# Kernel optimization log

Measured on AMD Instinct MI355X. Metric: run time of the kernel, lower is better.

## Reference

```python
import jax, jax.numpy as jnp
import numpy as np

B, T, U = 64, 512, 1024
TIME_STEP = 0.008

# Rieke cone phototransduction parameters (scaleFac = 1, values are final)
PR = dict(sigma=22.0, phi=22.0, eta=2000.0, beta=9.0, cgmp2cur=0.01,
          cgmphill=3.0, cdark=1.0, betaSlow=0.4, hillcoef=4.0,
          hillaffinity=0.5, gamma=10.0, gdark=20.0)


def setup_inputs() -> dict:
    key = jax.random.key(0)
    X = jax.random.uniform(key, (B, T, U), dtype=jnp.float32)  # light intensity >= 0
    inp = {"X_fun": X}
    for name, v in PR.items():
        inp[name] = jnp.full((1, U), v, dtype=jnp.float32)  # flax param shape (1, units)
    return inp


def reference(X_fun, sigma, phi, eta, beta, cgmp2cur, cgmphill, cdark,
              betaSlow, hillcoef, hillaffinity, gamma, gdark):
    # Derived constants (as in runRiekeModel preamble)
    darkCurrent = gdark ** cgmphill * cgmp2cur / 2
    gdark_e = (2 * darkCurrent / cgmp2cur) ** (1 / cgmphill)
    cur2ca = beta * cdark / darkCurrent
    smax = eta / phi * gdark_e * (1 + (cdark / hillaffinity) ** hillcoef)

    Bd, Td, Ud = X_fun.shape
    ones = jnp.ones((Bd, Ud), X_fun.dtype)
    g0 = gdark_e * ones
    s0 = gdark_e * eta / phi * ones
    c0 = cdark * ones
    cslow0 = cdark * ones
    r0 = X_fun[:, 0, :] * gamma / sigma
    p0 = (eta + r0) / phi

    def step(carry, x_prev):
        g, s, c, cslow, p, r = carry
        r_n = r + TIME_STEP * (-sigma * r) + gamma * x_prev
        p_n = p + TIME_STEP * (r + eta - phi * p)
        c_n = c + TIME_STEP * (cur2ca * cgmp2cur * g ** cgmphill
                               / (1 + cslow / cdark) - beta * c)
        cslow_n = cslow - TIME_STEP * (betaSlow * (cslow - c))
        s_n = smax / (1 + (c_n / hillaffinity) ** hillcoef)
        g_n = g + TIME_STEP * (s - p * g)
        return (g_n, s_n, c_n, cslow_n, p_n, r_n), g_n

    xs = jnp.moveaxis(X_fun[:, :-1, :], 1, 0)  # [T-1, B, U], step pnt uses X[:, pnt-1, :]
    _, g_seq = jax.lax.scan(step, (g0, s0, c0, cslow0, p0, r0), xs)
    # g[:, 0, :] stays zero in the original (loop starts at pnt=1)
    g = jnp.concatenate([jnp.zeros((Bd, 1, Ud), X_fun.dtype),
                         jnp.moveaxis(g_seq, 0, 1)], axis=1)
    return -(cgmp2cur * g ** cgmphill) / 2
```

## Files before the change

kernel.cpp:

```cpp
#include <hip/hip_runtime.h>
#include <math.h>


#define TT 512
#define UU 1024
#define UN 16
#define DTSTEP 0.008f

__device__ __forceinline__ void gload_lds(const float* g, float* l) {
    __builtin_amdgcn_global_load_lds(
        (__attribute__((address_space(1))) void*)(uintptr_t)g,
        (__attribute__((address_space(3))) void*)l, 4, 0, 0);
}

template <bool FAST>
__device__ __forceinline__ void run_chain(
    const float* __restrict__ xrow, float* __restrict__ orow,
    float* __restrict__ swave,
    int lane,
    float sigma, float phi, float eta, float beta, float cgmp2cur,
    float cgmphill, float cdark, float betaSlow, float hillcoef,
    float hillaff, float gam, float gdark)
{
    const float darkCurrent = powf(gdark, cgmphill) * cgmp2cur * 0.5f;
    const float gdark_e = powf(2.0f * darkCurrent / cgmp2cur, 1.0f / cgmphill);
    const float cur2ca = beta * cdark / darkCurrent;
    const float smax = eta / phi * gdark_e *
                       (1.0f + powf(cdark / hillaff, hillcoef));

    const float Ar   = 1.0f - DTSTEP * sigma;
    const float icd  = 1.0f / cdark;
    const float kc   = cur2ca * cgmp2cur;
    const float iha  = 1.0f / hillaff;
    const float outk = -0.5f * cgmp2cur;
    const float dtbs = DTSTEP * betaSlow;

    float g  = gdark_e;
    float s  = gdark_e * eta / phi;
    float c  = cdark;
    float cs = cdark;
    float r, p;
    {
        float x0 = xrow[0];
        r = x0 * gam / sigma;
        p = (eta + r) / phi;
    }
    float gp = FAST ? g * g * g : __powf(g, cgmphill);

    orow[0] = 0.0f;

    auto step = [&](float x, float& outv) {
        float rn  = fmaf(Ar, r, gam * x);
        float pn  = fmaf(DTSTEP, (r + eta) - phi * p, p);
        float den = fmaf(cs, icd, 1.0f);
        float cn  = fmaf(DTSTEP,
                         fmaf(-beta, c, kc * gp * __builtin_amdgcn_rcpf(den)),
                         c);
        float csn = fmaf(-dtbs, cs - c, cs);
        float sn;
        if (FAST) {
            float t2 = cn * iha;
            t2 *= t2;
            sn = smax * __builtin_amdgcn_rcpf(fmaf(t2, t2, 1.0f));
        } else {
            sn = smax / (1.0f + __powf(cn * iha, hillcoef));
        }
        float gn  = fmaf(DTSTEP, fmaf(-p, g, s), g);
        float gpn = FAST ? gn * gn * gn : __powf(gn, cgmphill);
        outv = outk * gpn;
        g = gn; s = sn; c = cn; cs = csn; p = pn; r = rn; gp = gpn;
    };

#pragma unroll
    for (int k = 0; k < UN; ++k)
        gload_lds(xrow + k * UU, swave + k * 64);

    const float* xst = xrow + UN * UU;
    float* op = orow + UU;

    for (int n = 0; n < TT / UN - 1; ++n) {
        if (n == 0) {
            asm volatile("s_waitcnt vmcnt(0)" ::: "memory");
        } else {
            asm volatile("s_waitcnt vmcnt(16)" ::: "memory");
        }
        __builtin_amdgcn_sched_barrier(0);
        const int p2 = (n & 1) * (UN * 64);
        float xa[UN];
#pragma unroll
        for (int k = 0; k < UN; ++k) xa[k] = swave[p2 + k * 64 + lane];
        __builtin_amdgcn_sched_barrier(0);
        const int q2 = ((n & 1) ^ 1) * (UN * 64);
#pragma unroll
        for (int k = 0; k < UN; ++k)
            gload_lds(xst + k * UU, swave + q2 + k * 64);
        __builtin_amdgcn_sched_barrier(0);
#pragma unroll
        for (int k = 0; k < UN; ++k) {
            float o;
            step(xa[k], o);
            op[k * UU] = o;
        }
        xst += UN * UU;
        op += UN * UU;
    }

    asm volatile("s_waitcnt vmcnt(16)" ::: "memory");
    __builtin_amdgcn_sched_barrier(0);
    {
        const int p2 = (31 & 1) * (UN * 64);
        float xa[UN];
#pragma unroll
        for (int k = 0; k < UN; ++k) xa[k] = swave[p2 + k * 64 + lane];
#pragma unroll
        for (int k = 0; k < UN - 1; ++k) {
            float o;
            step(xa[k], o);
            op[k * UU] = o;
        }
    }
}

__global__ __launch_bounds__(256, 1) void prfr_kernel(
    const float* __restrict__ X,
    const float* __restrict__ sigma_p, const float* __restrict__ phi_p,
    const float* __restrict__ eta_p,   const float* __restrict__ beta_p,
    const float* __restrict__ cgmp2cur_p, const float* __restrict__ cgmphill_p,
    const float* __restrict__ cdark_p, const float* __restrict__ betaSlow_p,
    const float* __restrict__ hillcoef_p, const float* __restrict__ hillaff_p,
    const float* __restrict__ gamma_p, const float* __restrict__ gdark_p,
    float* __restrict__ out, int total)
{
    __shared__ float smem[4][2][UN][64];

    const int idx = blockIdx.x * blockDim.x + threadIdx.x;
    if (idx >= total) return;
    const int u = idx & (UU - 1);
    const int b = idx >> 10;
    const int w = __builtin_amdgcn_readfirstlane(threadIdx.x >> 6);
    const int lane = threadIdx.x & 63;

    const float* xrow = X + (long)b * (TT * UU) + u;
    float* orow = out + (long)b * (TT * UU) + u;

    const float sigma = sigma_p[u], phi = phi_p[u], eta = eta_p[u];
    const float beta = beta_p[u], cgmp2cur = cgmp2cur_p[u];
    const float cgmphill = cgmphill_p[u], cdark = cdark_p[u];
    const float betaSlow = betaSlow_p[u], hillcoef = hillcoef_p[u];
    const float hillaff = hillaff_p[u], gam = gamma_p[u], gdark = gdark_p[u];

    float* swave = &smem[w][0][0][0];

    if (cgmphill == 3.0f && hillcoef == 4.0f) {
        run_chain<true>(xrow, orow, swave, lane, sigma, phi, eta, beta,
                        cgmp2cur, cgmphill, cdark, betaSlow, hillcoef,
                        hillaff, gam, gdark);
    } else {
        run_chain<false>(xrow, orow, swave, lane, sigma, phi, eta, beta,
                         cgmp2cur, cgmphill, cdark, betaSlow, hillcoef,
                         hillaff, gam, gdark);
    }
}

extern "C" void kernel_launch(void* const* d_in, const int* in_sizes, int n_in,
                              void* d_out, int out_size, void* d_ws, size_t ws_size,
                              hipStream_t stream)
{
    const float* X = (const float*)d_in[0];
    const int B = in_sizes[0] / (TT * UU);
    const int total = B * UU;
    const int block = 256;
    const int grid = (total + block - 1) / block;
    prfr_kernel<<<grid, block, 0, stream>>>(
        X,
        (const float*)d_in[1],  (const float*)d_in[2],  (const float*)d_in[3],
        (const float*)d_in[4],  (const float*)d_in[5],  (const float*)d_in[6],
        (const float*)d_in[7],  (const float*)d_in[8],  (const float*)d_in[9],
        (const float*)d_in[10], (const float*)d_in[11], (const float*)d_in[12],
        (float*)d_out, total);
}
```

Measured before the change: 257.3 us.

## Stage inputs with 16-byte LDS loads and fold step constants

The fast path now stages X into LDS with 16-byte global_load_lds transfers instead of 4-byte ones, remapping lanes so each wave fetches four timesteps per instruction. This cuts staging instructions per 16-step chunk from 16 to 4. The step's constants are pre-folded (P1, Ke, KC, C1), which shortens the serial dependency chain slightly. Output addressing uses a 32-bit unsigned offset, and the phase loop is unrolled by two. The generic path becomes a plain loop, and waitcnt counts still assume in-order completion alongside the stores.

```diff
diff --git a/kernel.cpp b/kernel.cpp
--- a/kernel.cpp
+++ b/kernel.cpp
@@ -4,20 +4,118 @@
 
 #define TT 512
 #define UU 1024
-#define UN 16
 #define DTSTEP 0.008f
 
-__device__ __forceinline__ void gload_lds(const float* g, float* l) {
+__device__ __forceinline__ void gload16(const float* g, float* l) {
     __builtin_amdgcn_global_load_lds(
         (__attribute__((address_space(1))) void*)(uintptr_t)g,
-        (__attribute__((address_space(3))) void*)l, 4, 0, 0);
-}
-
-template <bool FAST>
-__device__ __forceinline__ void run_chain(
-    const float* __restrict__ xrow, float* __restrict__ orow,
-    float* __restrict__ swave,
-    int lane,
+        (__attribute__((address_space(3))) void*)l, 16, 0, 0);
+}
+
+__device__ __forceinline__ void run_fast(
+    const float* __restrict__ xrow, float* __restrict__ out, unsigned ob,
+    const float* gstage, float* __restrict__ wlds, int lane,
+    float sigma, float phi, float eta, float beta, float cgmp2cur,
+    float cdark, float betaSlow, float hillaff, float gam, float gdark)
+{
+    const float darkCurrent = gdark * gdark * gdark * cgmp2cur * 0.5f;
+    const float gdark_e = gdark;
+    const float cur2ca = beta * cdark / darkCurrent;
+    const float ha2 = (cdark / hillaff) * (cdark / hillaff);
+    const float smax = eta / phi * gdark_e * (1.0f + ha2 * ha2);
+
+    const float Ar   = 1.0f - DTSTEP * sigma;
+    const float P1   = 1.0f - DTSTEP * phi;
+    const float Ke   = DTSTEP * eta;
+    const float icd  = 1.0f / cdark;
+    const float KC   = DTSTEP * cur2ca * cgmp2cur;
+    const float C1   = 1.0f - DTSTEP * beta;
+    const float dtbs = DTSTEP * betaSlow;
+    const float iha  = 1.0f / hillaff;
+    const float outk = -0.5f * cgmp2cur;
+
+    float g  = gdark_e;
+    float s  = gdark_e * eta / phi;
+    float c  = cdark;
+    float cs = cdark;
+    float x0 = xrow[0];
+    float r  = x0 * gam / sigma;
+    float p  = (eta + r) / phi;
+    float gp = g * g * g;
+
+    out[ob - UU] = 0.0f;
+
+#pragma unroll
+    for (int j = 0; j < 4; ++j) {
+        gload16(gstage, wlds + j * 256);
+        gstage += 4 * UU;
+    }
+
+    auto step = [&](float x, float& o) {
+        float rn  = fmaf(Ar, r, gam * x);
+        float pn  = fmaf(P1, p, fmaf(DTSTEP, r, Ke));
+        float den = fmaf(cs, icd, 1.0f);
+        float rd  = __builtin_amdgcn_rcpf(den);
+        float cn  = fmaf(KC, gp * rd, C1 * c);
+        float csn = fmaf(-dtbs, cs - c, cs);
+        float t2  = cn * iha;
+        t2 *= t2;
+        float sn  = smax * __builtin_amdgcn_rcpf(fmaf(t2, t2, 1.0f));
+        float gn  = fmaf(DTSTEP, fmaf(-p, g, s), g);
+        float gpn = gn * gn * gn;
+        o = outk * gpn;
+        g = gn; s = sn; c = cn; cs = csn; p = pn; r = rn; gp = gpn;
+    };
+
+    auto phase = [&](int buf, bool dostage, bool first) {
+        if (first) asm volatile("s_waitcnt vmcnt(0)" ::: "memory");
+        else       asm volatile("s_waitcnt vmcnt(16)" ::: "memory");
+        __builtin_amdgcn_sched_barrier(0);
+        if (dostage) {
+#pragma unroll
+            for (int j = 0; j < 4; ++j) {
+                gload16(gstage, wlds + (buf ^ 1) * 1024 + j * 256);
+                gstage += 4 * UU;
+            }
+        }
+        __builtin_amdgcn_sched_barrier(0);
+        const float* rb = wlds + buf * 1024 + lane;
+        float xa[16];
+#pragma unroll
+        for (int k = 0; k < 16; ++k) xa[k] = rb[k * 64];
+        __builtin_amdgcn_sched_barrier(0);
+#pragma unroll
+        for (int k = 0; k < 16; ++k) {
+            float o;
+            step(xa[k], o);
+            out[ob + (unsigned)(k * UU)] = o;
+        }
+        ob += 16u * UU;
+    };
+
+    phase(0, true, true);
+    for (int n2 = 0; n2 < 15; ++n2) {
+        phase(1, true, false);
+        phase(0, true, false);
+    }
+    asm volatile("s_waitcnt vmcnt(16)" ::: "memory");
+    __builtin_amdgcn_sched_barrier(0);
+    {
+        const float* rb = wlds + 1024 + lane;
+        float xa[16];
+#pragma unroll
+        for (int k = 0; k < 16; ++k) xa[k] = rb[k * 64];
+#pragma unroll
+        for (int k = 0; k < 15; ++k) {
+            float o;
+            step(xa[k], o);
+            out[ob + (unsigned)(k * UU)] = o;
+        }
+    }
+}
+
+__device__ void run_generic(
+    const float* __restrict__ xrow, float* __restrict__ out, unsigned ob,
     float sigma, float phi, float eta, float beta, float cgmp2cur,
     float cgmphill, float cdark, float betaSlow, float hillcoef,
     float hillaff, float gam, float gdark)
@@ -27,97 +125,26 @@
     const float cur2ca = beta * cdark / darkCurrent;
     const float smax = eta / phi * gdark_e *
                        (1.0f + powf(cdark / hillaff, hillcoef));
-
-    const float Ar   = 1.0f - DTSTEP * sigma;
-    const float icd  = 1.0f / cdark;
-    const float kc   = cur2ca * cgmp2cur;
-    const float iha  = 1.0f / hillaff;
-    const float outk = -0.5f * cgmp2cur;
-    const float dtbs = DTSTEP * betaSlow;
-
     float g  = gdark_e;
     float s  = gdark_e * eta / phi;
     float c  = cdark;
     float cs = cdark;
-    float r, p;
-    {
-        float x0 = xrow[0];
-        r = x0 * gam / sigma;
-        p = (eta + r) / phi;
-    }
-    float gp = FAST ? g * g * g : __powf(g, cgmphill);
-
-    orow[0] = 0.0f;
-
-    auto step = [&](float x, float& outv) {
-        float rn  = fmaf(Ar, r, gam * x);
-        float pn  = fmaf(DTSTEP, (r + eta) - phi * p, p);
-        float den = fmaf(cs, icd, 1.0f);
-        float cn  = fmaf(DTSTEP,
-                         fmaf(-beta, c, kc * gp * __builtin_amdgcn_rcpf(den)),
-                         c);
-        float csn = fmaf(-dtbs, cs - c, cs);
-        float sn;
-        if (FAST) {
-            float t2 = cn * iha;
-            t2 *= t2;
-            sn = smax * __builtin_amdgcn_rcpf(fmaf(t2, t2, 1.0f));
-        } else {
-            sn = smax / (1.0f + __powf(cn * iha, hillcoef));
-        }
-        float gn  = fmaf(DTSTEP, fmaf(-p, g, s), g);
-        float gpn = FAST ? gn * gn * gn : __powf(gn, cgmphill);
-        outv = outk * gpn;
-        g = gn; s = sn; c = cn; cs = csn; p = pn; r = rn; gp = gpn;
-    };
-
-#pragma unroll
-    for (int k = 0; k < UN; ++k)
-        gload_lds(xrow + k * UU, swave + k * 64);
-
-    const float* xst = xrow + UN * UU;
-    float* op = orow + UU;
-
-    for (int n = 0; n < TT / UN - 1; ++n) {
-        if (n == 0) {
-            asm volatile("s_waitcnt vmcnt(0)" ::: "memory");
-        } else {
-            asm volatile("s_waitcnt vmcnt(16)" ::: "memory");
-        }
-        __builtin_amdgcn_sched_barrier(0);
-        const int p2 = (n & 1) * (UN * 64);
-        float xa[UN];
-#pragma unroll
-        for (int k = 0; k < UN; ++k) xa[k] = swave[p2 + k * 64 + lane];
-        __builtin_amdgcn_sched_barrier(0);
-        const int q2 = ((n & 1) ^ 1) * (UN * 64);
-#pragma unroll
-        for (int k = 0; k < UN; ++k)
-            gload_lds(xst + k * UU, swave + q2 + k * 64);
-        __builtin_amdgcn_sched_barrier(0);
-#pragma unroll
-        for (int k = 0; k < UN; ++k) {
-            float o;
-            step(xa[k], o);
-            op[k * UU] = o;
-        }
-        xst += UN * UU;
-        op += UN * UU;
-    }
-
-    asm volatile("s_waitcnt vmcnt(16)" ::: "memory");
-    __builtin_amdgcn_sched_barrier(0);
-    {
-        const int p2 = (31 & 1) * (UN * 64);
-        float xa[UN];
-#pragma unroll
-        for (int k = 0; k < UN; ++k) xa[k] = swave[p2 + k * 64 + lane];
-#pragma unroll
-        for (int k = 0; k < UN - 1; ++k) {
-            float o;
-            step(xa[k], o);
-            op[k * UU] = o;
-        }
+    float x0 = xrow[0];
+    float r  = x0 * gam / sigma;
+    float p  = (eta + r) / phi;
+    out[ob - UU] = 0.0f;
+    for (int t = 1; t < TT; ++t) {
+        float x  = xrow[(t - 1) * UU];
+        float rn = r + DTSTEP * (-sigma * r) + gam * x;
+        float pn = p + DTSTEP * (r + eta - phi * p);
+        float cn = c + DTSTEP * (cur2ca * cgmp2cur * powf(g, cgmphill)
+                                 / (1.0f + cs / cdark) - beta * c);
+        float csn = cs - DTSTEP * (betaSlow * (cs - c));
+        float sn  = smax / (1.0f + powf(cn / hillaff, hillcoef));
+        float gn  = g + DTSTEP * (s - p * g);
+        out[ob + (unsigned)((t - 1) * UU)] =
+            -(cgmp2cur * powf(gn, cgmphill)) * 0.5f;
+        g = gn; s = sn; c = cn; cs = csn; p = pn; r = rn;
     }
 }
 
@@ -131,7 +158,7 @@
     const float* __restrict__ gamma_p, const float* __restrict__ gdark_p,
     float* __restrict__ out, int total)
 {
-    __shared__ float smem[4][2][UN][64];
+    __shared__ float smem[4][2][16][64];
 
     const int idx = blockIdx.x * blockDim.x + threadIdx.x;
     if (idx >= total) return;
@@ -140,8 +167,11 @@
     const int w = __builtin_amdgcn_readfirstlane(threadIdx.x >> 6);
     const int lane = threadIdx.x & 63;
 
-    const float* xrow = X + (long)b * (TT * UU) + u;
-    float* orow = out + (long)b * (TT * UU) + u;
+    const float* xrow = X + (size_t)b * (TT * UU) + u;
+    const unsigned ob = (unsigned)b * (TT * UU) + UU + (unsigned)u;
+
+    const int uq = (u - lane) + 4 * (lane & 15);
+    const float* gstage = X + ((size_t)b * TT + (lane >> 4)) * UU + uq;
 
     const float sigma = sigma_p[u], phi = phi_p[u], eta = eta_p[u];
     const float beta = beta_p[u], cgmp2cur = cgmp2cur_p[u];
@@ -149,16 +179,13 @@
     const float betaSlow = betaSlow_p[u], hillcoef = hillcoef_p[u];
     const float hillaff = hillaff_p[u], gam = gamma_p[u], gdark = gdark_p[u];
 
-    float* swave = &smem[w][0][0][0];
-
     if (cgmphill == 3.0f && hillcoef == 4.0f) {
-        run_chain<true>(xrow, orow, swave, lane, sigma, phi, eta, beta,
-                        cgmp2cur, cgmphill, cdark, betaSlow, hillcoef,
-                        hillaff, gam, gdark);
+        run_fast(xrow, out, ob, gstage, &smem[w][0][0][0], lane,
+                 sigma, phi, eta, beta, cgmp2cur, cdark, betaSlow,
+                 hillaff, gam, gdark);
     } else {
-        run_chain<false>(xrow, orow, swave, lane, sigma, phi, eta, beta,
-                         cgmp2cur, cgmphill, cdark, betaSlow, hillcoef,
-                         hillaff, gam, gdark);
+        run_generic(xrow, out, ob, sigma, phi, eta, beta, cgmp2cur,
+                    cgmphill, cdark, betaSlow, hillcoef, hillaff, gam, gdark);
     }
 }
 
```

Result: no change. 255.6 us (-0.7%).
